# Performance work log

Measured on AMD Instinct MI355X. Metric: run time of the kernel, lower is better.

Reference implementation:

```python
import jax, jax.numpy as jnp
import numpy as np


def setup_inputs() -> dict:
    key = jax.random.key(0)
    k1, k2 = jax.random.split(key)
    B, S, H, D = 4, 4096, 2048, 3
    hidden_states = jax.random.normal(k1, (B, S, H), dtype=jnp.float32)
    theta = jax.random.normal(k2, (D, H), dtype=jnp.float32)  # routing_params stacked [D,H]
    return {"hidden_states": hidden_states, "theta": theta}


def reference(hidden_states, theta):
    B, S, H = hidden_states.shape
    D = theta.shape[0]
    k = max(1, int(S * (1.0 / D)))  # tokens kept per depth step

    # Per-depth gemv scoring + sigmoid, all depths at once: [B,S,D]
    scores = jax.nn.sigmoid(jnp.einsum('bsh,dh->bsd', hidden_states, theta))

    depth = jnp.zeros((B, S), dtype=jnp.int32)
    active = jnp.ones((B, S), dtype=bool)
    bidx = jnp.arange(B)[:, None]  # [B,1] for batched scatter
    neg_inf = jnp.float32(-jnp.inf)

    for r in range(D):  # D is small and fixed (3)
        masked = jnp.where(active, scores[:, :, r], neg_inf)
        _, idx = jax.lax.top_k(masked, k)  # [B,k]
        depth = depth.at[bidx, idx].set(r + 1)
        step_mask = jnp.zeros((B, S), dtype=bool).at[bidx, idx].set(True)
        active = active & step_mask

    depth = jnp.where(depth == 0, 1, depth)

    # Balancing loss: note the original applies sigmoid twice (scores_list is
    # post-sigmoid, then compute_balancing_loss sigmoids again). batchmean over D.
    probs = jax.nn.sigmoid(scores).mean(axis=(0, 1))  # [D]
    target = jnp.float32(1.0 / D)
    balancing_loss = jnp.sum(target * (jnp.log(target) - jnp.log(probs))) / D

    # masks list: [ones, final_active, final_active] stacked as [D,B,S]
    masks = jnp.stack([jnp.ones((B, S), dtype=bool) if r == 0 else active
                       for r in range(D)])
    return depth, balancing_loss, masks
```

## Files before the change

kernel.cpp:

```cpp
#include <hip/hip_runtime.h>
#include <math.h>

#define BB 4
#define SS 4096
#define HH 2048
#define DD 3
#define KK 1365
#define ONEBITS 0x3f800000u

__global__ __launch_bounds__(256) void score_kernel(
    const float* __restrict__ hs, const float* __restrict__ theta,
    float* __restrict__ scores0, double* __restrict__ partials,
    float* __restrict__ m0)
{
    const long gid = (long)blockIdx.x * 256 + threadIdx.x;
    if (gid < (long)BB * SS) m0[gid] = 1.0f;

    const int wave = threadIdx.x >> 6;
    const int lane = threadIdx.x & 63;
    const long token = (long)blockIdx.x * 4 + wave;

    const float4* row = reinterpret_cast<const float4*>(hs + token * HH);
    const float4* t0p = reinterpret_cast<const float4*>(theta);
    const float4* t1p = reinterpret_cast<const float4*>(theta + HH);
    const float4* t2p = reinterpret_cast<const float4*>(theta + 2 * HH);

    double a0 = 0.0, a1 = 0.0, a2 = 0.0;
#pragma unroll
    for (int j = 0; j < HH / 256; ++j) {
        const int v = j * 64 + lane;
        float4 h  = row[v];
        float4 x0 = t0p[v];
        float4 x1 = t1p[v];
        float4 x2 = t2p[v];
        a0 += (double)h.x * x0.x + (double)h.y * x0.y + (double)h.z * x0.z + (double)h.w * x0.w;
        a1 += (double)h.x * x1.x + (double)h.y * x1.y + (double)h.z * x1.z + (double)h.w * x1.w;
        a2 += (double)h.x * x2.x + (double)h.y * x2.y + (double)h.z * x2.z + (double)h.w * x2.w;
    }
#pragma unroll
    for (int off = 32; off; off >>= 1) {
        a0 += __shfl_down(a0, off);
        a1 += __shfl_down(a1, off);
        a2 += __shfl_down(a2, off);
    }

    __shared__ double wpart[4][DD];
    if (lane == 0) {
        float x0 = (float)a0, x1 = (float)a1, x2 = (float)a2;
        float s0 = 1.0f / (1.0f + expf(-x0));
        float s1 = 1.0f / (1.0f + expf(-x1));
        float s2 = 1.0f / (1.0f + expf(-x2));
        scores0[token] = s0;
        wpart[wave][0] = (double)(1.0f / (1.0f + expf(-s0)));
        wpart[wave][1] = (double)(1.0f / (1.0f + expf(-s1)));
        wpart[wave][2] = (double)(1.0f / (1.0f + expf(-s2)));
    }
    __syncthreads();
    if (threadIdx.x < DD) {
        const int d = threadIdx.x;
        partials[(long)blockIdx.x * DD + d] =
            wpart[0][d] + wpart[1][d] + wpart[2][d] + wpart[3][d];
    }
}

__global__ __launch_bounds__(1024) void select_kernel(
    const float* __restrict__ scores0, const double* __restrict__ partials,
    float* __restrict__ out)
{
    const int tid  = threadIdx.x;
    const int lane = tid & 63;
    const int wid  = tid >> 6;
    const int blk  = blockIdx.x;

    if (blk == 12) {
        double a0 = 0.0, a1 = 0.0, a2 = 0.0;
        for (int i = tid; i < 4096; i += 1024) {
            a0 += partials[(long)i * DD + 0];
            a1 += partials[(long)i * DD + 1];
            a2 += partials[(long)i * DD + 2];
        }
#pragma unroll
        for (int off = 32; off; off >>= 1) {
            a0 += __shfl_down(a0, off);
            a1 += __shfl_down(a1, off);
            a2 += __shfl_down(a2, off);
        }
        __shared__ double shl[DD][16];
        if (lane == 0) { shl[0][wid] = a0; shl[1][wid] = a1; shl[2][wid] = a2; }
        __syncthreads();
        if (tid == 0) {
            double p0 = 0, p1 = 0, p2 = 0;
            for (int w = 0; w < 16; ++w) { p0 += shl[0][w]; p1 += shl[1][w]; p2 += shl[2][w]; }
            const double n = (double)BB * SS;
            p0 /= n; p1 /= n; p2 /= n;
            const double t = 1.0 / 3.0;
            out[(long)BB * SS] = (float)((t * (log(t) - log(p0)) +
                                          t * (log(t) - log(p1)) +
                                          t * (log(t) - log(p2))) / 3.0);
        }
        return;
    }

    const int b = blk / 3, plane = blk % 3;
    const float* rowp = scores0 + (long)b * SS;

    __shared__ unsigned wsum[16];
    __shared__ __align__(16) unsigned su[SS];
    __shared__ unsigned whist[16 * 256];
    __shared__ unsigned wtot[4];
    __shared__ unsigned sbin, skk;

    uint4 uu = reinterpret_cast<const uint4*>(rowp)[tid];

    unsigned vstar = ONEBITS;
    unsigned e0 = (uu.x == vstar), e1 = (uu.y == vstar),
             e2 = (uu.z == vstar), e3 = (uu.w == vstar);
    unsigned cnt = e0 + e1 + e2 + e3;

    unsigned inc = cnt;
#pragma unroll
    for (int off = 1; off < 64; off <<= 1) {
        unsigned t = __shfl_up(inc, off);
        if (lane >= off) inc += t;
    }
    if (lane == 63) wsum[wid] = inc;
    __syncthreads();
    if (wid == 0) {
        unsigned wv = (lane < 16) ? wsum[lane] : 0;
#pragma unroll
        for (int off = 1; off < 16; off <<= 1) {
            unsigned t = __shfl_up(wv, off);
            if (lane >= off) wv += t;
        }
        if (lane < 16) wsum[lane] = wv;
    }
    __syncthreads();
    unsigned p     = inc - cnt + (wid > 0 ? wsum[wid - 1] : 0);
    unsigned total = wsum[15];
    unsigned rem   = KK;

    if (total < KK) {
        for (int i = tid; i < SS; i += 1024) su[i] = __float_as_uint(rowp[i]);
        unsigned prefix = 0, maskbits = 0, kk = KK;
        for (int pass = 0; pass < 4; ++pass) {
            const int shift = 24 - 8 * pass;
            for (int i = tid; i < 16 * 256; i += 1024) whist[i] = 0;
            __syncthreads();
            for (int i = tid; i < SS; i += 1024) {
                unsigned u = su[i];
                if ((u & maskbits) == prefix)
                    atomicAdd(&whist[(wid << 8) + ((u >> shift) & 255u)], 1u);
            }
            __syncthreads();
            unsigned val = 0, s = 0;
            if (tid < 256) {
                for (int w = 0; w < 16; ++w) val += whist[(w << 8) + tid];
                s = val;
#pragma unroll
                for (int off = 1; off < 64; off <<= 1) {
                    unsigned t = __shfl_down(s, off);
                    if (lane + off < 64) s += t;
                }
                if (lane == 0) wtot[wid] = s;
            }
            __syncthreads();
            if (tid < 256) {
                unsigned cge = s;
                for (int w = wid + 1; w < 4; ++w) cge += wtot[w];
                unsigned cgt = cge - val;
                if (cgt < kk && cge >= kk) { sbin = (unsigned)tid; skk = kk - cgt; }
            }
            __syncthreads();
            prefix   |= (sbin << shift);
            maskbits |= (255u << shift);
            kk = skk;
        }
        vstar = prefix;
        rem   = kk;
        e0 = (uu.x == vstar); e1 = (uu.y == vstar);
        e2 = (uu.z == vstar); e3 = (uu.w == vstar);
        cnt = e0 + e1 + e2 + e3;
        inc = cnt;
#pragma unroll
        for (int off = 1; off < 64; off <<= 1) {
            unsigned t = __shfl_up(inc, off);
            if (lane >= off) inc += t;
        }
        __syncthreads();
        if (lane == 63) wsum[wid] = inc;
        __syncthreads();
        if (wid == 0) {
            unsigned wv = (lane < 16) ? wsum[lane] : 0;
#pragma unroll
            for (int off = 1; off < 16; off <<= 1) {
                unsigned t = __shfl_up(wv, off);
                if (lane >= off) wv += t;
            }
            if (lane < 16) wsum[lane] = wv;
        }
        __syncthreads();
        p = inc - cnt + (wid > 0 ? wsum[wid - 1] : 0);
    }

    const bool sel0 = (uu.x > vstar) || (e0 && p < rem); p += e0;
    const bool sel1 = (uu.y > vstar) || (e1 && p < rem); p += e1;
    const bool sel2 = (uu.z > vstar) || (e2 && p < rem); p += e2;
    const bool sel3 = (uu.w > vstar) || (e3 && p < rem);

    if (plane == 0) {
        float4 dv = make_float4(sel0 ? 3.0f : 1.0f, sel1 ? 3.0f : 1.0f,
                                sel2 ? 3.0f : 1.0f, sel3 ? 3.0f : 1.0f);
        reinterpret_cast<float4*>(out + (long)b * SS)[tid] = dv;
    } else {
        float* m = out + (long)BB * SS + 1 + (long)plane * BB * SS + (long)b * SS;
        const int base = tid * 4;
        m[base + 0] = sel0 ? 1.0f : 0.0f;
        m[base + 1] = sel1 ? 1.0f : 0.0f;
        m[base + 2] = sel2 ? 1.0f : 0.0f;
        m[base + 3] = sel3 ? 1.0f : 0.0f;
    }
}

extern "C" void kernel_launch(void* const* d_in, const int* in_sizes, int n_in,
                              void* d_out, int out_size, void* d_ws, size_t ws_size,
                              hipStream_t stream) {
    const float* hs    = (const float*)d_in[0];
    const float* theta = (const float*)d_in[1];
    float* out = (float*)d_out;

    float*  scores0  = (float*)d_ws;
    double* partials = (double*)((char*)d_ws + (size_t)BB * SS * 4);
    float*  m0       = out + (long)BB * SS + 1;

    score_kernel <<<dim3(BB * SS / 4), dim3(256),  0, stream>>>(hs, theta, scores0, partials, m0);
    select_kernel<<<dim3(13),          dim3(1024), 0, stream>>>(scores0, partials, out);
}
```

Before: 31.39 us.

## Stage theta in LDS and score four tokens per wave

The scoring kernel now copies the 3x2048 theta matrix into shared memory once per block. Each wave then computes dot products for four tokens, reusing every theta load across four hidden-state rows and keeping more independent row loads in flight. The grid shrinks to 1024 blocks, and the loss reduction in the select kernel reads correspondingly fewer partials. In exchange it uses more registers (12 double accumulators), 24KB of LDS per block, pays a theta prologue per block, and has fewer blocks to hide memory latency.

Measured after the change: 39.04 us. 24.4% more time.

```diff
diff --git a/kernel.cpp b/kernel.cpp
--- a/kernel.cpp
+++ b/kernel.cpp
@@ -7,57 +7,92 @@
 #define DD 3
 #define KK 1365
 #define ONEBITS 0x3f800000u
+#define TPW 4
+#define NWAVE 4
+#define SBLOCKS (BB * SS / (TPW * NWAVE * 64 / 64) / NWAVE)
 
 __global__ __launch_bounds__(256) void score_kernel(
     const float* __restrict__ hs, const float* __restrict__ theta,
     float* __restrict__ scores0, double* __restrict__ partials,
     float* __restrict__ m0)
 {
-    const long gid = (long)blockIdx.x * 256 + threadIdx.x;
+    __shared__ __align__(16) float th[DD * HH];
+    __shared__ double wpart[NWAVE][DD];
+
+    const int tid = threadIdx.x;
+
+    {
+        const float4* src = reinterpret_cast<const float4*>(theta);
+        float4* dst = reinterpret_cast<float4*>(th);
+#pragma unroll
+        for (int i = 0; i < 6; ++i) dst[tid + 256 * i] = src[tid + 256 * i];
+    }
+
+    const long gid = (long)blockIdx.x * 256 + tid;
     if (gid < (long)BB * SS) m0[gid] = 1.0f;
 
-    const int wave = threadIdx.x >> 6;
-    const int lane = threadIdx.x & 63;
-    const long token = (long)blockIdx.x * 4 + wave;
-
-    const float4* row = reinterpret_cast<const float4*>(hs + token * HH);
-    const float4* t0p = reinterpret_cast<const float4*>(theta);
-    const float4* t1p = reinterpret_cast<const float4*>(theta + HH);
-    const float4* t2p = reinterpret_cast<const float4*>(theta + 2 * HH);
-
-    double a0 = 0.0, a1 = 0.0, a2 = 0.0;
+    __syncthreads();
+
+    const int wave = tid >> 6;
+    const int lane = tid & 63;
+    const int w    = blockIdx.x * NWAVE + wave;
+    const long tok0 = (long)w * TPW;
+
+    const float4* r0 = reinterpret_cast<const float4*>(hs + (tok0 + 0) * HH);
+    const float4* r1 = reinterpret_cast<const float4*>(hs + (tok0 + 1) * HH);
+    const float4* r2 = reinterpret_cast<const float4*>(hs + (tok0 + 2) * HH);
+    const float4* r3 = reinterpret_cast<const float4*>(hs + (tok0 + 3) * HH);
+    const float4* t0p = reinterpret_cast<const float4*>(th);
+    const float4* t1p = reinterpret_cast<const float4*>(th + HH);
+    const float4* t2p = reinterpret_cast<const float4*>(th + 2 * HH);
+
+    double acc[TPW][DD] = {};
 #pragma unroll
     for (int j = 0; j < HH / 256; ++j) {
         const int v = j * 64 + lane;
-        float4 h  = row[v];
-        float4 x0 = t0p[v];
-        float4 x1 = t1p[v];
-        float4 x2 = t2p[v];
-        a0 += (double)h.x * x0.x + (double)h.y * x0.y + (double)h.z * x0.z + (double)h.w * x0.w;
-        a1 += (double)h.x * x1.x + (double)h.y * x1.y + (double)h.z * x1.z + (double)h.w * x1.w;
-        a2 += (double)h.x * x2.x + (double)h.y * x2.y + (double)h.z * x2.z + (double)h.w * x2.w;
-    }
-#pragma unroll
-    for (int off = 32; off; off >>= 1) {
-        a0 += __shfl_down(a0, off);
-        a1 += __shfl_down(a1, off);
-        a2 += __shfl_down(a2, off);
-    }
-
-    __shared__ double wpart[4][DD];
+        const float4 x0 = t0p[v];
+        const float4 x1 = t1p[v];
+        const float4 x2 = t2p[v];
+        const float4 h0 = r0[v];
+        const float4 h1 = r1[v];
+        const float4 h2 = r2[v];
+        const float4 h3 = r3[v];
+#define ACCUM(t, h)                                                                           \
+        acc[t][0] += (double)h.x * x0.x + (double)h.y * x0.y + (double)h.z * x0.z + (double)h.w * x0.w; \
+        acc[t][1] += (double)h.x * x1.x + (double)h.y * x1.y + (double)h.z * x1.z + (double)h.w * x1.w; \
+        acc[t][2] += (double)h.x * x2.x + (double)h.y * x2.y + (double)h.z * x2.z + (double)h.w * x2.w;
+        ACCUM(0, h0) ACCUM(1, h1) ACCUM(2, h2) ACCUM(3, h3)
+#undef ACCUM
+    }
+
+#pragma unroll
+    for (int t = 0; t < TPW; ++t)
+#pragma unroll
+        for (int d = 0; d < DD; ++d)
+#pragma unroll
+            for (int off = 32; off; off >>= 1)
+                acc[t][d] += __shfl_down(acc[t][d], off);
+
     if (lane == 0) {
-        float x0 = (float)a0, x1 = (float)a1, x2 = (float)a2;
-        float s0 = 1.0f / (1.0f + expf(-x0));
-        float s1 = 1.0f / (1.0f + expf(-x1));
-        float s2 = 1.0f / (1.0f + expf(-x2));
-        scores0[token] = s0;
-        wpart[wave][0] = (double)(1.0f / (1.0f + expf(-s0)));
-        wpart[wave][1] = (double)(1.0f / (1.0f + expf(-s1)));
-        wpart[wave][2] = (double)(1.0f / (1.0f + expf(-s2)));
-    }
-    __syncthreads();
-    if (threadIdx.x < DD) {
-        const int d = threadIdx.x;
+        double ss0 = 0.0, ss1 = 0.0, ss2 = 0.0;
+#pragma unroll
+        for (int t = 0; t < TPW; ++t) {
+            const float x0 = (float)acc[t][0];
+            const float x1 = (float)acc[t][1];
+            const float x2 = (float)acc[t][2];
+            const float s0 = 1.0f / (1.0f + expf(-x0));
+            const float s1 = 1.0f / (1.0f + expf(-x1));
+            const float s2 = 1.0f / (1.0f + expf(-x2));
+            scores0[tok0 + t] = s0;
+            ss0 += (double)(1.0f / (1.0f + expf(-s0)));
+            ss1 += (double)(1.0f / (1.0f + expf(-s1)));
+            ss2 += (double)(1.0f / (1.0f + expf(-s2)));
+        }
+        wpart[wave][0] = ss0; wpart[wave][1] = ss1; wpart[wave][2] = ss2;
+    }
+    __syncthreads();
+    if (tid < DD) {
+        const int d = tid;
         partials[(long)blockIdx.x * DD + d] =
             wpart[0][d] + wpart[1][d] + wpart[2][d] + wpart[3][d];
     }
@@ -74,7 +109,7 @@
 
     if (blk == 12) {
         double a0 = 0.0, a1 = 0.0, a2 = 0.0;
-        for (int i = tid; i < 4096; i += 1024) {
+        for (int i = tid; i < 1024; i += 1024) {
             a0 += partials[(long)i * DD + 0];
             a1 += partials[(long)i * DD + 1];
             a2 += partials[(long)i * DD + 2];
@@ -232,6 +267,6 @@
     double* partials = (double*)((char*)d_ws + (size_t)BB * SS * 4);
     float*  m0       = out + (long)BB * SS + 1;
 
-    score_kernel <<<dim3(BB * SS / 4), dim3(256),  0, stream>>>(hs, theta, scores0, partials, m0);
-    select_kernel<<<dim3(13),          dim3(1024), 0, stream>>>(scores0, partials, out);
+    score_kernel <<<dim3(1024), dim3(256),  0, stream>>>(hs, theta, scores0, partials, m0);
+    select_kernel<<<dim3(13),   dim3(1024), 0, stream>>>(scores0, partials, out);
 }
```
